# Optimization experiments

Hardware: AMD Instinct MI355X
Metric: run time of the kernel (lower is better)

The kernel has to match this reference:

```python
import jax, jax.numpy as jnp
import numpy as np

N, E = 30000, 240000          # nodes, edges per view
IN, D, OUT = 512, 128, 64      # in_dim, hidden_dim, out_dim
V, BLK, H, DM = 2, 2, 2, 64    # num_view, blk_size, num_heads, gate max-pool dim
NEG_ATT, NEG_OUT = 0.2, 0.01   # leaky_relu slopes (attention / outer)


def setup_inputs() -> dict:
    key = jax.random.key(0)
    ks = jax.random.split(key, 12)
    s = 0.05
    f32 = jnp.float32
    return {
        "ft": jax.random.normal(ks[0], (N, IN), f32),
        "src": jax.random.randint(ks[1], (V, E), 0, N, jnp.int32),
        "dst": jax.random.randint(ks[2], (V, E), 0, N, jnp.int32),
        "W_proj": jax.random.normal(ks[3], (IN, D), f32) * s,
        "W_embed": jax.random.normal(ks[4], (D, D), f32) * s,
        "a_l": jax.random.normal(ks[5], (V, BLK, H, D), f32) * s,
        "a_r": jax.random.normal(ks[6], (V, BLK, H, D), f32) * s,
        "Wv": jax.random.normal(ks[7], (V, BLK, H, D, D), f32) * s,
        "Wgm": jax.random.normal(ks[8], (V, BLK, D, DM), f32) * s,
        "Wgate": jax.random.normal(ks[9], (V, BLK, 2 * D + DM, H), f32) * s,
        "b_gate": jnp.zeros((V, BLK, H), f32),
        "W_tran": jax.random.normal(ks[10], (2 * D + DM and (D + V * H * D), OUT), f32) * s if False else jax.random.normal(ks[10], (D + V * H * D, OUT), f32) * s,
        "b_tran": jnp.zeros((OUT,), f32),
    }


def _seg_sum(x, idx):
    return jax.ops.segment_sum(x, idx, num_segments=N)


def _cgaan_layer(v, z, s_idx, d_idx, al, ar, wv, wgm, wgate, bg, merge):
    # v: [N,D] values, z: [N,D] attention features ('proj_z')
    # Multi-head attention logits: e_ij = leaky_relu(a_l.z_src + a_r.z_dst)  [E,H]
    logit_l = jnp.einsum("nd,hd->nh", z, al)
    logit_r = jnp.einsum("nd,hd->nh", z, ar)
    e = jax.nn.leaky_relu(logit_l[s_idx] + logit_r[d_idx], NEG_ATT)
    # edge softmax over incoming edges of each dst node
    m = jax.ops.segment_max(e, d_idx, num_segments=N)          # [N,H]
    ex = jnp.exp(e - m[d_idx])
    denom = _seg_sum(ex, d_idx)                                 # [N,H]
    alpha = ex / denom[d_idx]                                   # [E,H]
    # per-head value projection and weighted aggregation
    wvn = jnp.einsum("nd,hde->nhe", v, wv)                      # [N,H,D]
    agg = _seg_sum(alpha[:, :, None] * wvn[s_idx], d_idx)       # [N,H,D]
    # GaAN-style gate: sigmoid(FC([x_i, mean_j v_j, max_j (v_j Wgm)])) -> per-head scalar
    deg = _seg_sum(jnp.ones((s_idx.shape[0],), v.dtype), d_idx)  # [N]
    mean_n = _seg_sum(v[s_idx], d_idx) / jnp.maximum(deg, 1.0)[:, None]
    mx = jax.ops.segment_max((v @ wgm)[s_idx], d_idx, num_segments=N)
    mx = jnp.where(deg[:, None] > 0, mx, 0.0)                   # isolated nodes -> 0
    g = jax.nn.sigmoid(jnp.concatenate([v, mean_n, mx], -1) @ wgate + bg)  # [N,H]
    agg = g[:, :, None] * agg
    if merge == "mean":
        return agg.mean(axis=1)                                 # [N,D]
    return agg.reshape(agg.shape[0], -1)                        # cat -> [N,H*D]


def reference(ft, src, dst, W_proj, W_embed, a_l, a_r, Wv, Wgm, Wgate, b_gate, W_tran, b_tran):
    proj = ft @ W_proj                                          # [N,D]
    cur = [proj for _ in range(V)]
    for i in range(BLK):
        merge = "mean" if i < BLK - 1 else "cat"
        nxt = []
        for j in range(V):
            z = cur[j] @ W_embed
            h = _cgaan_layer(cur[j], z, src[j], dst[j], a_l[j, i], a_r[j, i],
                             Wv[j, i], Wgm[j, i], Wgate[j, i], b_gate[j, i], merge)
            nxt.append(jax.nn.leaky_relu(h, NEG_OUT))
        cur = nxt
    h = jnp.concatenate([proj] + cur, axis=-1)                  # [N, D+V*H*D]
    return h @ W_tran + b_tran
```

## Files before the change

### kernel.cpp

```cpp
#include <hip/hip_runtime.h>
#include <hip/hip_bf16.h>
#include <math.h>

#define NN 30000
#define EE 240000
#define IN_DIM 512
#define DD 128
#define OUTD 64
#define NV 2
#define NBLK 2
#define NH 2
#define DMM 64
#define NEG_ATT 0.2f
#define NEG_OUT 0.01f
#define CH 1024
#define NCH ((NN + CH - 1) / CH)

typedef __attribute__((ext_vector_type(8))) short bf16x8;
typedef __attribute__((ext_vector_type(4))) float f32x4;
typedef __attribute__((ext_vector_type(4))) unsigned short us4;
typedef __attribute__((ext_vector_type(8))) unsigned short us8;

#define OFF_PROJVM 0
#define OFF_WV     131072
#define OFF_WGM    262144
#define OFF_TRAN   278528
#define WT_TOTAL   319488

__device__ __forceinline__ unsigned split_bf(float x) {
  unsigned u = __float_as_uint(x);
  unsigned hb = (u + 0x7FFFu + ((u >> 16) & 1u)) >> 16;
  float hf = __uint_as_float(hb << 16);
  float lo = x - hf;
  unsigned ul = __float_as_uint(lo);
  unsigned lb = (ul + 0x7FFFu + ((ul >> 16) & 1u)) >> 16;
  return hb | (lb << 16);
}
__device__ __forceinline__ unsigned short f2bf(float x) {
  unsigned u = __float_as_uint(x);
  return (unsigned short)((u + 0x7FFFu + ((u >> 16) & 1u)) >> 16);
}
__device__ __forceinline__ float bf2f(unsigned short u) {
  return __uint_as_float((unsigned)u << 16);
}
__device__ __forceinline__ void gload16(void* lds, const void* g) {
  __builtin_amdgcn_global_load_lds((const __attribute__((address_space(1))) unsigned int*)g,
                                   (__attribute__((address_space(3))) unsigned int*)lds, 16, 0, 0);
}

__global__ __launch_bounds__(256) void kA_deg_prepw(const int* __restrict__ dst, int* __restrict__ deg,
                                                    const float* __restrict__ W_embed,
                                                    const float* __restrict__ a_l, const float* __restrict__ a_r,
                                                    const float* __restrict__ Wp, const float* __restrict__ Wgm,
                                                    float* __restrict__ Bl, float* __restrict__ Br,
                                                    float* __restrict__ wf) {
  int b = blockIdx.x;
  if (b < 1875) {
    int e = b * 256 + threadIdx.x;
    if (e < NV * EE) atomicAdd(&deg[(e / EE) * NN + dst[e]], 1);
    return;
  }
  int pb = b - 1875;
  if (pb < 256) {
    int idx = pb * 256 + threadIdx.x;
    int j = idx >> 15, k = (idx >> 6) & 511, n = idx & 63;
    const float* wp = Wp + (size_t)k * DD;
    const float* wg = Wgm + (size_t)(j * NBLK + 0) * DD * DMM + n;
    float s = 0.f;
    for (int e = 0; e < DD; e++) s += wp[e] * wg[(size_t)e * DMM];
    wf[idx] = s;
  } else {
    int idx = (pb - 256) * 256 + threadIdx.x;
    if (idx >= NV * NBLK * DD * NH) return;
    int h = idx & 1, dd = (idx >> 1) & 127, lv = idx >> 8;
    const float* w = W_embed + dd * DD;
    const float* al = a_l + (lv * NH + h) * DD;
    const float* ar = a_r + (lv * NH + h) * DD;
    float sl = 0.f, sr = 0.f;
    for (int e = 0; e < DD; e++) { float we = w[e]; sl += we * al[e]; sr += we * ar[e]; }
    Bl[idx] = sl; Br[idx] = sr;
  }
}

__global__ __launch_bounds__(256) void kB_scan1_wsplit(const int* __restrict__ deg, int* __restrict__ partial,
                                                       const float* __restrict__ Wp, const float* __restrict__ wf,
                                                       const float* __restrict__ Wv, const float* __restrict__ Wgm,
                                                       const float* __restrict__ Wt,
                                                       unsigned short* __restrict__ hi,
                                                       unsigned short* __restrict__ lo) {
  int b = blockIdx.x;
  if (b < 60) {
    int view = b / NCH, ch = b % NCH;
    const int* d = deg + view * NN + ch * CH;
    int rem = min(CH, NN - ch * CH);
    int t = threadIdx.x;
    int s = 0;
    for (int i = t; i < rem; i += 256) s += d[i];
    for (int k = 32; k; k >>= 1) s += __shfl_xor(s, k);
    __shared__ int wsum[4];
    if ((t & 63) == 0) wsum[t >> 6] = s;
    __syncthreads();
    if (t == 0) partial[b] = wsum[0] + wsum[1] + wsum[2] + wsum[3];
    return;
  }
  int wb = b - 60;
  const int pre[11] = {0, 256, 384, 512, 640, 768, 896, 1024, 1056, 1088, 1248};
  int y = 0;
  while (y < 10 && wb >= pre[y + 1]) y++;
  int bx = wb - pre[y];
  const float* src; int K, N; size_t doff;
  if (y == 0)      { src = Wp;                      K = 512; N = 128; doff = OFF_PROJVM; }
  else if (y <= 2) { int j = y - 1; src = wf + (size_t)j * 512 * 64; K = 512; N = 64; doff = OFF_PROJVM + (size_t)(128 + j * 64) * 512; }
  else if (y <= 6) { int lv = y - 3; src = Wv + (size_t)lv * 32768;  K = 256; N = 128; doff = OFF_WV + (size_t)lv * 32768; }
  else if (y <= 8) { int j = y - 7; src = Wgm + (size_t)(j * NBLK + 1) * 8192; K = 128; N = 64; doff = OFF_WGM + (size_t)j * 8192; }
  else             { src = Wt;                      K = 640; N = 64;  doff = OFF_TRAN; }
  int idx = bx * 256 + threadIdx.x;
  if (idx >= K * N) return;
  int n = idx / K, k = idx % K;
  int tk = k >> 6, g = (k >> 3) & 7, j2 = k & 7;
  int ks = (tk << 6) | ((g ^ (n & 7)) << 3) | j2;
  unsigned p = split_bf(src[(size_t)k * N + n]);
  hi[doff + (size_t)n * K + ks] = (unsigned short)(p & 0xFFFFu);
  lo[doff + (size_t)n * K + ks] = (unsigned short)(p >> 16);
}

__global__ void k_scan2(const int* __restrict__ partial, int* __restrict__ chunkoff, int* __restrict__ off) {
  if (threadIdx.x == 0 && blockIdx.x == 0) {
    for (int v = 0; v < NV; v++) {
      int acc = 0;
      for (int c = 0; c < NCH; c++) { chunkoff[v * NCH + c] = acc; acc += partial[v * NCH + c]; }
      off[v * (NN + 1) + NN] = acc;
    }
  }
}

__global__ __launch_bounds__(256) void k_scan3(const int* __restrict__ deg, const int* __restrict__ chunkoff,
                                               int* __restrict__ off) {
  int b = blockIdx.x, view = b / NCH, ch = b % NCH;
  int base = ch * CH;
  const int* d = deg + view * NN;
  int* o = off + view * (NN + 1);
  int t = threadIdx.x, lane = t & 63, w = t >> 6;
  int i0 = base + t * 4;
  int x0 = 0, x1 = 0, x2 = 0, x3 = 0;
  if (i0 + 3 < NN) { int4 q = *(const int4*)(d + i0); x0 = q.x; x1 = q.y; x2 = q.z; x3 = q.w; }
  else {
    if (i0     < NN) x0 = d[i0];
    if (i0 + 1 < NN) x1 = d[i0 + 1];
    if (i0 + 2 < NN) x2 = d[i0 + 2];
  }
  int tot = x0 + x1 + x2 + x3;
  int incl = tot;
  for (int k = 1; k < 64; k <<= 1) { int y = __shfl_up(incl, k); if (lane >= k) incl += y; }
  __shared__ int wt[4];
  if (lane == 63) wt[w] = incl;
  __syncthreads();
  int wexcl = 0;
  for (int k = 0; k < w; k++) wexcl += wt[k];
  int excl = chunkoff[b] + wexcl + incl - tot;
  if (i0     < NN) o[i0]     = excl;
  if (i0 + 1 < NN) o[i0 + 1] = excl + x0;
  if (i0 + 2 < NN) o[i0 + 2] = excl + x0 + x1;
  if (i0 + 3 < NN) o[i0 + 3] = excl + x0 + x1 + x2;
}

__global__ __launch_bounds__(256) void k_fill(const int* __restrict__ src, const int* __restrict__ dst,
                                              const int* __restrict__ off, int* __restrict__ cursor,
                                              int* __restrict__ csr_src) {
  int e = blockIdx.x * 256 + threadIdx.x;
  if (e >= NV * EE) return;
  int view = e / EE;
  int d = dst[e];
  int p = atomicAdd(&cursor[view * NN + d], 1);
  csr_src[view * EE + off[view * (NN + 1) + d] + p] = src[e];
}

__global__ __launch_bounds__(256) void k_llr(const unsigned short* __restrict__ p0,
                                             const unsigned short* __restrict__ p1, int ps,
                                             const float* __restrict__ Bl0, const float* __restrict__ Br0,
                                             const float* __restrict__ Bl1, const float* __restrict__ Br1,
                                             const float* __restrict__ Wg0, const float* __restrict__ Wg1,
                                             float4* __restrict__ lq, float2* __restrict__ lr) {
  int lane = threadIdx.x & 63, wid = threadIdx.x >> 6;
  int n = blockIdx.x * 4 + wid;
  int k = lane * 2;
  unsigned a = *(const unsigned*)(p0 + (size_t)n * ps + k);
  unsigned b = *(const unsigned*)(p1 + (size_t)n * ps + k);
  float ax = bf2f((unsigned short)a), ay = bf2f((unsigned short)(a >> 16));
  float bx = bf2f((unsigned short)b), by = bf2f((unsigned short)(b >> 16));
  float r[12];
  r[0]  = ax * Bl0[k * 2]     + ay * Bl0[k * 2 + 2];
  r[1]  = ax * Bl0[k * 2 + 1] + ay * Bl0[k * 2 + 3];
  r[2]  = ax * Br0[k * 2]     + ay * Br0[k * 2 + 2];
  r[3]  = ax * Br0[k * 2 + 1] + ay * Br0[k * 2 + 3];
  r[4]  = ax * Wg0[(128 + k) * 2]     + ay * Wg0[(129 + k) * 2];
  r[5]  = ax * Wg0[(128 + k) * 2 + 1] + ay * Wg0[(129 + k) * 2 + 1];
  r[6]  = bx * Bl1[k * 2]     + by * Bl1[k * 2 + 2];
  r[7]  = bx * Bl1[k * 2 + 1] + by * Bl1[k * 2 + 3];
  r[8]  = bx * Br1[k * 2]     + by * Br1[k * 2 + 2];
  r[9]  = bx * Br1[k * 2 + 1] + by * Br1[k * 2 + 3];
  r[10] = bx * Wg1[(128 + k) * 2]     + by * Wg1[(129 + k) * 2];
  r[11] = bx * Wg1[(128 + k) * 2 + 1] + by * Wg1[(129 + k) * 2 + 1];
  for (int s = 32; s; s >>= 1)
#pragma unroll
    for (int q = 0; q < 12; q++) r[q] += __shfl_xor(r[q], s);
  if (lane == 0) {
    lq[n] = make_float4(r[0], r[1], r[4], r[5]);
    lr[n] = make_float2(r[2], r[3]);
    lq[NN + n] = make_float4(r[6], r[7], r[10], r[11]);
    lr[NN + n] = make_float2(r[8], r[9]);
  }
}

__global__ __launch_bounds__(256) void k_edge(const int* __restrict__ off_, const int* __restrict__ csr_,
                                              const float4* __restrict__ lq_, const float2* __restrict__ lr_,
                                              const unsigned short* __restrict__ pk_, long viewStride,
                                              int ps, int vmoff0, int vmstep,
                                              const float* __restrict__ Wg_, const float* __restrict__ bg_,
                                              unsigned short* __restrict__ S_) {
  int view = blockIdx.y;
  const int* off = off_ + view * (NN + 1);
  const int* csr = csr_ + (size_t)view * EE;
  const float4* lq = lq_ + (size_t)view * NN;
  const float2* lrp = lr_ + (size_t)view * NN;
  const unsigned short* pk = pk_ + (size_t)view * viewStride;
  int vmoff = vmoff0 + view * vmstep;
  const float* Wg = Wg_ + (size_t)view * NBLK * (2 * DD + DMM) * NH;
  const float* bg = bg_ + view * NBLK * NH;
  unsigned short* S = S_ + (size_t)view * NN * 256;

  int lane = threadIdx.x & 63, wid = threadIdx.x >> 6;
  int n = blockIdx.x * 4 + wid;
  int e0 = off[n], nb = off[n + 1] - e0;
  int half = lane >> 5, hl = lane & 31;
  if (nb == 0) {
    us4 z4 = {0, 0, 0, 0};
    *(us4*)(S + (size_t)n * 256 + half * 128 + 4 * hl) = z4;
    return;
  }
  float2 lrn = lrp[n];
  float sa0[4] = {0.f, 0.f, 0.f, 0.f}, sa1[4] = {0.f, 0.f, 0.f, 0.f};
  float d0 = 0.f, d1 = 0.f, tm0 = 0.f, tm1 = 0.f, vm0 = -INFINITY, vm1 = -INFINITY;
  for (int base = 0; base < nb; base += 64) {
    int i = base + lane;
    float w0 = 0.f, w1 = 0.f; int sidx = 0;
    if (i < nb) {
      sidx = csr[e0 + i];
      float4 qq = lq[sidx];
      float x0 = qq.x + lrn.x, x1 = qq.y + lrn.y;
      x0 = (x0 > 0.f) ? x0 : NEG_ATT * x0;
      x1 = (x1 > 0.f) ? x1 : NEG_ATT * x1;
      w0 = __expf(x0); w1 = __expf(x1);
      d0 += w0; d1 += w1; tm0 += qq.z; tm1 += qq.w;
    }
    int cnt = min(64, nb - base);
    int steps = (cnt + 1) >> 1;
    int j = half;
    int se = __shfl(sidx, j);
    float wa = __shfl(w0, j), wb = __shfl(w1, j);
    const unsigned short* rp = pk + (size_t)se * ps;
    us4 vq = *(const us4*)(rp + 4 * hl);
    unsigned mu = *(const unsigned*)(rp + vmoff + 2 * hl);
    bool ok = (j < cnt);
    for (int s = 0; s < steps; s++) {
      int j1 = 2 * (s + 1) + half;
      int jc = min(j1, 63);
      int se1 = __shfl(sidx, jc);
      float wa1 = __shfl(w0, jc), wb1 = __shfl(w1, jc);
      const unsigned short* rp1 = pk + (size_t)se1 * ps;
      us4 vq1 = *(const us4*)(rp1 + 4 * hl);
      unsigned mu1 = *(const unsigned*)(rp1 + vmoff + 2 * hl);
      float v0 = bf2f(vq[0]), v1 = bf2f(vq[1]), v2 = bf2f(vq[2]), v3 = bf2f(vq[3]);
      sa0[0] += wa * v0; sa0[1] += wa * v1; sa0[2] += wa * v2; sa0[3] += wa * v3;
      sa1[0] += wb * v0; sa1[1] += wb * v1; sa1[2] += wb * v2; sa1[3] += wb * v3;
      float mv0 = ok ? bf2f((unsigned short)mu) : -INFINITY;
      float mv1 = ok ? bf2f((unsigned short)(mu >> 16)) : -INFINITY;
      vm0 = fmaxf(vm0, mv0); vm1 = fmaxf(vm1, mv1);
      vq = vq1; mu = mu1; wa = wa1; wb = wb1; ok = (j1 < cnt);
    }
  }
#pragma unroll
  for (int k = 0; k < 4; k++) {
    sa0[k] += __shfl_xor(sa0[k], 32);
    sa1[k] += __shfl_xor(sa1[k], 32);
  }
  vm0 = fmaxf(vm0, __shfl_xor(vm0, 32));
  vm1 = fmaxf(vm1, __shfl_xor(vm1, 32));
  for (int s = 32; s; s >>= 1) { d0 += __shfl_xor(d0, s); d1 += __shfl_xor(d1, s); }
  unsigned vnu = *(const unsigned*)(pk + (size_t)n * ps + 2 * lane);
  float vnx = bf2f((unsigned short)vnu), vny = bf2f((unsigned short)(vnu >> 16));
  float im = 1.f / (float)nb;
  float p0 = vnx * Wg[(2 * lane) * 2]     + vny * Wg[(2 * lane + 1) * 2]     + tm0 * im;
  float p1 = vnx * Wg[(2 * lane) * 2 + 1] + vny * Wg[(2 * lane + 1) * 2 + 1] + tm1 * im;
  if (half == 1) {
    p0 += vm0 * Wg[(256 + 2 * hl) * 2]     + vm1 * Wg[(256 + 2 * hl + 1) * 2];
    p1 += vm0 * Wg[(256 + 2 * hl) * 2 + 1] + vm1 * Wg[(256 + 2 * hl + 1) * 2 + 1];
  }
  for (int s = 32; s; s >>= 1) { p0 += __shfl_xor(p0, s); p1 += __shfl_xor(p1, s); }
  float g0 = 1.f / (1.f + __expf(-(p0 + bg[0])));
  float g1 = 1.f / (1.f + __expf(-(p1 + bg[1])));
  float q0 = g0 / d0, q1 = g1 / d1;
  us4 o4;
  if (half == 0) {
    o4[0] = f2bf(sa0[0] * q0); o4[1] = f2bf(sa0[1] * q0);
    o4[2] = f2bf(sa0[2] * q0); o4[3] = f2bf(sa0[3] * q0);
  } else {
    o4[0] = f2bf(sa1[0] * q1); o4[1] = f2bf(sa1[1] * q1);
    o4[2] = f2bf(sa1[2] * q1); o4[3] = f2bf(sa1[3] * q1);
  }
  *(us4*)(S + (size_t)n * 256 + half * 128 + 4 * hl) = o4;
}

struct GB {
  const void* A[4];
  unsigned long long bofs[4];
  float* C[4];
  unsigned short* P[4];
  int ldc[4];
  int pldc[4];
};

template <int BN, bool ABF>
__global__ __launch_bounds__(256) void gemm_mfma(
    GB gb, const unsigned short* __restrict__ Bth, const unsigned short* __restrict__ Btl,
    int lda, int ldb, int M, int K,
    const float* __restrict__ bias, float fs, int flags) {
  constexpr int NSUB = BN / 32;
  constexpr int CPW = BN / 32;
  __shared__ __align__(16) unsigned short Ah[64][64];
  __shared__ __align__(16) unsigned short Bh[BN][64], Bl[BN][64];
  const int z = blockIdx.z, xb = blockIdx.x;
  const float* __restrict__ Af = (const float*)gb.A[z];
  const unsigned short* __restrict__ Ab = (const unsigned short*)gb.A[z];
  float* __restrict__ C = gb.C[z];
  unsigned short* __restrict__ P = gb.P[z];
  const int ldc = gb.ldc[z], pldc = gb.pldc[z];
  const size_t bofs = gb.bofs[z];
  const int t = threadIdx.x;
  const int lane = t & 63, wv = t >> 6;
  const int lm = lane & 15, lg = lane >> 4;
  const int m0w = (wv & 1) * 32, n0w = (wv >> 1) * (BN / 2);
  const int row0 = xb * 64;
  f32x4 acc[2][NSUB];
#pragma unroll
  for (int ms = 0; ms < 2; ms++)
#pragma unroll
    for (int ns = 0; ns < NSUB; ns++) acc[ms][ns] = (f32x4)0.f;

  float4 apre[2][2];
  const int ar_ = t >> 3, ag_ = t & 7;

  auto loadA = [&](int k0) {
    if constexpr (!ABF) {
#pragma unroll
      for (int q = 0; q < 2; q++) {
        int rr = row0 + q * 32 + ar_;
        if (rr < M) {
          const float* p = Af + (size_t)rr * lda + k0 + ag_ * 8;
          apre[q][0] = *(const float4*)p;
          apre[q][1] = *(const float4*)(p + 4);
        } else {
          apre[q][0] = make_float4(0.f, 0.f, 0.f, 0.f);
          apre[q][1] = make_float4(0.f, 0.f, 0.f, 0.f);
        }
      }
    }
  };
  auto storeA = [&]() {
    if constexpr (!ABF) {
#pragma unroll
      for (int q = 0; q < 2; q++) {
        int r = q * 32 + ar_;
        us8 h8;
        float vals[8] = {apre[q][0].x, apre[q][0].y, apre[q][0].z, apre[q][0].w,
                         apre[q][1].x, apre[q][1].y, apre[q][1].z, apre[q][1].w};
#pragma unroll
        for (int e = 0; e < 8; e++) h8[e] = f2bf(vals[e]);
        int c = (ag_ ^ (r & 7)) << 3;
        *(us8*)&Ah[r][c] = h8;
      }
    }
  };
  auto stageA_bf = [&](int k0) {
    if constexpr (ABF) {
#pragma unroll
      for (int q = 0; q < 2; q++) {
        int r = q * 32 + ar_;
        int rr = min(row0 + r, M - 1);
        int scg = ag_ ^ (r & 7);
        gload16((char*)&Ah[0][0] + q * 4096 + t * 16,
                Ab + (size_t)rr * lda + k0 + scg * 8);
      }
    }
  };
  auto stageB = [&](int k0) {
#pragma unroll
    for (int q = 0; q < CPW; q++) {
      int chunk = wv * CPW + q;
      int o = chunk * 1024 + lane * 16;
      int n = o >> 7;
      int pq = (o >> 4) & 7;
      size_t gofs = bofs + (size_t)n * ldb + k0 + pq * 8;
      gload16((char*)&Bh[0][0] + o, Bth + gofs);
      gload16((char*)&Bl[0][0] + o, Btl + gofs);
    }
  };

  loadA(0);
  for (int k0 = 0; k0 < K; k0 += 64) {
    if constexpr (ABF) stageA_bf(k0); else storeA();
    stageB(k0);
    __syncthreads();
    if constexpr (!ABF) { if (k0 + 64 < K) loadA(k0 + 64); }
#pragma unroll
    for (int kc = 0; kc < 2; kc++) {
      bf16x8 afh[2], bfh[NSUB], bfl[NSUB];
#pragma unroll
      for (int ms = 0; ms < 2; ms++) {
        int R = m0w + ms * 16 + lm;
        int c = (((kc * 4 + lg) ^ (R & 7)) << 3);
        afh[ms] = *(const bf16x8*)&Ah[R][c];
      }
#pragma unroll
      for (int ns = 0; ns < NSUB; ns++) {
        int R = n0w + ns * 16 + lm;
        int c = (((kc * 4 + lg) ^ (R & 7)) << 3);
        bfh[ns] = *(const bf16x8*)&Bh[R][c];
        bfl[ns] = *(const bf16x8*)&Bl[R][c];
      }
#pragma unroll
      for (int ms = 0; ms < 2; ms++)
#pragma unroll
        for (int ns = 0; ns < NSUB; ns++) {
          acc[ms][ns] = __builtin_amdgcn_mfma_f32_16x16x32_bf16(afh[ms], bfl[ns], acc[ms][ns], 0, 0, 0);
          acc[ms][ns] = __builtin_amdgcn_mfma_f32_16x16x32_bf16(afh[ms], bfh[ns], acc[ms][ns], 0, 0, 0);
        }
    }
    __syncthreads();
  }
#pragma unroll
  for (int ms = 0; ms < 2; ms++)
#pragma unroll
    for (int ns = 0; ns < NSUB; ns++)
#pragma unroll
      for (int j = 0; j < 4; j++) {
        int row = row0 + m0w + ms * 16 + lg * 4 + j;
        if (row >= M) continue;
        int col = n0w + ns * 16 + lm;
        float val = acc[ms][ns][j] * fs;
        if (bias) val += bias[col];
        if (flags & 2) val = (val > 0.f) ? val : NEG_OUT * val;
        if (C) C[(size_t)row * ldc + col] = val;
        if (P) P[(size_t)row * pldc + col] = f2bf(val);
      }
}

extern "C" void kernel_launch(void* const* d_in, const int* in_sizes, int n_in,
                              void* d_out, int out_size, void* d_ws, size_t ws_size,
                              hipStream_t stream) {
  const float* ft      = (const float*)d_in[0];
  const int*   src     = (const int*)  d_in[1];
  const int*   dst     = (const int*)  d_in[2];
  const float* W_proj  = (const float*)d_in[3];
  const float* W_embed = (const float*)d_in[4];
  const float* a_l     = (const float*)d_in[5];
  const float* a_r     = (const float*)d_in[6];
  const float* Wv      = (const float*)d_in[7];
  const float* Wgm     = (const float*)d_in[8];
  const float* Wgate   = (const float*)d_in[9];
  const float* b_gate  = (const float*)d_in[10];
  const float* W_tran  = (const float*)d_in[11];
  const float* b_tran  = (const float*)d_in[12];
  float* out = (float*)d_out;
  char* ws = (char*)d_ws;
  (void)in_sizes; (void)n_in; (void)out_size; (void)ws_size;

  size_t o = 0;
  auto take = [&](size_t bytes) { size_t r = o; o += (bytes + 255) & ~(size_t)255; return r; };
  int*   deg     = (int*)(ws + take((size_t)NV * NN * 4));
  int*   cursor  = (int*)(ws + take((size_t)NV * NN * 4));
  int*   csr_off = (int*)(ws + take((size_t)NV * (NN + 1) * 4));
  int*   csr_src = (int*)(ws + take((size_t)NV * EE * 4));
  int*   partial = (int*)(ws + take((size_t)NV * NCH * 4));
  int*   chunkoff= (int*)(ws + take((size_t)NV * NCH * 4));
  float* Bl      = (float*)(ws + take((size_t)NV * NBLK * DD * NH * 4));
  float* Br      = (float*)(ws + take((size_t)NV * NBLK * DD * NH * 4));
  float* wf      = (float*)(ws + take((size_t)NV * 512 * 64 * 4));
  unsigned short* whi = (unsigned short*)(ws + take((size_t)WT_TOTAL * 2));
  unsigned short* wlo = (unsigned short*)(ws + take((size_t)WT_TOTAL * 2));
  float* h       = (float*)(ws + take((size_t)NN * 640 * 4));
  unsigned short* pk0 = (unsigned short*)(ws + take((size_t)NN * 256 * 2));
  unsigned short* pk1 = (unsigned short*)(ws + take((size_t)NV * NN * 192 * 2));
  unsigned short* Sbf = (unsigned short*)(ws + take((size_t)NV * NN * 256 * 2));
  float4* lqb    = (float4*)(ws + take((size_t)NV * NN * 16));
  float2* lrb    = (float2*)(ws + take((size_t)NV * NN * 8));

  const int HSTR = 640;

  hipMemsetAsync(deg, 0, (size_t)(((size_t)NV * NN * 4 + 255) & ~(size_t)255) + (size_t)NV * NN * 4, stream);
  kA_deg_prepw<<<2135, 256, 0, stream>>>(dst, deg, W_embed, a_l, a_r, W_proj, Wgm, Bl, Br, wf);
  kB_scan1_wsplit<<<1308, 256, 0, stream>>>(deg, partial, W_proj, wf, Wv, Wgm, W_tran, whi, wlo);
  k_scan2<<<1, 64, 0, stream>>>(partial, chunkoff, csr_off);
  k_scan3<<<NV * NCH, 256, 0, stream>>>(deg, chunkoff, csr_off);
  k_fill<<<(NV * EE + 255) / 256, 256, 0, stream>>>(src, dst, csr_off, cursor, csr_src);

  const int GM = (NN + 63) / 64;

  {
    GB gb = {};
    gb.A[0] = ft; gb.A[1] = ft;
    gb.bofs[0] = OFF_PROJVM; gb.bofs[1] = OFF_PROJVM + (size_t)128 * 512;
    gb.C[0] = h;  gb.ldc[0] = HSTR;
    gb.P[0] = pk0;       gb.pldc[0] = 256;
    gb.P[1] = pk0 + 128; gb.pldc[1] = 256;
    gemm_mfma<128, false><<<dim3(GM, 1, 2), 256, 0, stream>>>(gb, whi, wlo, IN_DIM, 512, NN, 512,
                                                              nullptr, 1.f, 0);
  }

  k_llr<<<NN / 4, 256, 0, stream>>>(pk0, pk0, 256,
                                    Bl + 0 * 256, Br + 0 * 256, Bl + 2 * 256, Br + 2 * 256,
                                    Wgate, Wgate + (size_t)NBLK * 320 * NH,
                                    lqb, lrb);
  k_edge<<<dim3(NN / 4, 2), 256, 0, stream>>>(csr_off, csr_src, lqb, lrb,
                                              pk0, 0L, 256, 128, 64,
                                              Wgate, b_gate, Sbf);
  {
    GB gb = {};
    for (int j = 0; j < 2; j++) {
      gb.A[j] = Sbf + (size_t)j * NN * 256;
      gb.bofs[j] = OFF_WV + (size_t)(j * 2) * 32768;
      gb.P[j] = pk1 + (size_t)j * NN * 192;
      gb.pldc[j] = 192;
    }
    gemm_mfma<128, true><<<dim3(GM, 1, 2), 256, 0, stream>>>(gb, whi, wlo, 256, 256, NN, 256,
                                                             nullptr, 0.5f, 2);
  }
  {
    GB gb = {};
    for (int j = 0; j < 2; j++) {
      gb.A[j] = pk1 + (size_t)j * NN * 192;
      gb.bofs[j] = OFF_WGM + (size_t)j * 8192;
      gb.P[j] = pk1 + (size_t)j * NN * 192 + 128;
      gb.pldc[j] = 192;
    }
    gemm_mfma<64, true><<<dim3(GM, 1, 2), 256, 0, stream>>>(gb, whi, wlo, 192, 128, NN, 128,
                                                            nullptr, 1.f, 0);
  }
  k_llr<<<NN / 4, 256, 0, stream>>>(pk1, pk1 + (size_t)NN * 192, 192,
                                    Bl + 1 * 256, Br + 1 * 256, Bl + 3 * 256, Br + 3 * 256,
                                    Wgate + 640, Wgate + (size_t)NBLK * 640 + 640,
                                    lqb, lrb);
  k_edge<<<dim3(NN / 4, 2), 256, 0, stream>>>(csr_off, csr_src, lqb, lrb,
                                              pk1, (long)NN * 192, 192, 128, 0,
                                              Wgate + 640, b_gate + NH, Sbf);
  {
    GB gb = {};
    for (int z = 0; z < 4; z++) {
      int j = z >> 1, hd = z & 1;
      gb.A[z] = Sbf + (size_t)j * NN * 256 + hd * 128;
      gb.bofs[z] = OFF_WV + (size_t)(j * 2 + 1) * 32768 + hd * 128;
      gb.C[z] = h + 128 + z * 128;
      gb.ldc[z] = HSTR;
    }
    gemm_mfma<128, true><<<dim3(GM, 1, 4), 256, 0, stream>>>(gb, whi, wlo, 256, 256, NN, 128,
                                                             nullptr, 1.f, 2);
  }
  {
    GB gb = {};
    gb.A[0] = h; gb.bofs[0] = OFF_TRAN; gb.C[0] = out; gb.ldc[0] = OUTD;
    gemm_mfma<64, false><<<dim3(GM, 1, 1), 256, 0, stream>>>(gb, whi, wlo, HSTR, 640, NN, 640,
                                                             b_tran, 1.f, 0);
  }
}
```

Before: 325.1 us.

## Fold CSR fill and logit kernels into GEMM launches and drop scan2

The single-thread chunk-offset scan kernel is removed. Each k_scan3 block now sums the partial counts of the preceding chunks itself and writes the final total. The CSR fill work is folded into extra blocks of the first projection GEMM, and the second attention-logit pass into extra blocks of the Wgm GEMM, selected by flag bits and block index. This cuts kernel launches and the serialization between small kernels, so the independent work can overlap with GEMM tiles. The edge kernel also precomputes byte offsets for the gathered rows to shave address arithmetic, at the cost of a larger GEMM kernel signature and early-exit branches in its blocks.

```diff
diff --git a/kernel.cpp b/kernel.cpp
--- a/kernel.cpp
+++ b/kernel.cpp
@@ -46,6 +46,55 @@
 __device__ __forceinline__ void gload16(void* lds, const void* g) {
   __builtin_amdgcn_global_load_lds((const __attribute__((address_space(1))) unsigned int*)g,
                                    (__attribute__((address_space(3))) unsigned int*)lds, 16, 0, 0);
+}
+
+struct AUX {
+  const int* fsrc; const int* fdst; const int* foff; int* fcur; int* fcsr;
+  const unsigned short* lp0; const unsigned short* lp1; int lps;
+  const float *lBl0, *lBr0, *lBl1, *lBr1, *lWg0, *lWg1;
+  float4* llq; float2* llr;
+};
+
+__device__ void fill_body(int fb, int t, const AUX& a) {
+  int e = fb * 256 + t;
+  if (e >= NV * EE) return;
+  int view = e / EE;
+  int d = a.fdst[e];
+  int p = atomicAdd(&a.fcur[view * NN + d], 1);
+  a.fcsr[view * EE + a.foff[view * (NN + 1) + d] + p] = a.fsrc[e];
+}
+
+__device__ void llr_body(int lid, int t, const AUX& a) {
+  int lane = t & 63, wid = t >> 6;
+  int n = lid * 4 + wid;
+  if (n >= NN) return;
+  int k = lane * 2;
+  unsigned av = *(const unsigned*)(a.lp0 + (size_t)n * a.lps + k);
+  unsigned bv = *(const unsigned*)(a.lp1 + (size_t)n * a.lps + k);
+  float ax = bf2f((unsigned short)av), ay = bf2f((unsigned short)(av >> 16));
+  float bx = bf2f((unsigned short)bv), by = bf2f((unsigned short)(bv >> 16));
+  float r[12];
+  r[0]  = ax * a.lBl0[k * 2]     + ay * a.lBl0[k * 2 + 2];
+  r[1]  = ax * a.lBl0[k * 2 + 1] + ay * a.lBl0[k * 2 + 3];
+  r[2]  = ax * a.lBr0[k * 2]     + ay * a.lBr0[k * 2 + 2];
+  r[3]  = ax * a.lBr0[k * 2 + 1] + ay * a.lBr0[k * 2 + 3];
+  r[4]  = ax * a.lWg0[(128 + k) * 2]     + ay * a.lWg0[(129 + k) * 2];
+  r[5]  = ax * a.lWg0[(128 + k) * 2 + 1] + ay * a.lWg0[(129 + k) * 2 + 1];
+  r[6]  = bx * a.lBl1[k * 2]     + by * a.lBl1[k * 2 + 2];
+  r[7]  = bx * a.lBl1[k * 2 + 1] + by * a.lBl1[k * 2 + 3];
+  r[8]  = bx * a.lBr1[k * 2]     + by * a.lBr1[k * 2 + 2];
+  r[9]  = bx * a.lBr1[k * 2 + 1] + by * a.lBr1[k * 2 + 3];
+  r[10] = bx * a.lWg1[(128 + k) * 2]     + by * a.lWg1[(129 + k) * 2];
+  r[11] = bx * a.lWg1[(128 + k) * 2 + 1] + by * a.lWg1[(129 + k) * 2 + 1];
+  for (int s = 32; s; s >>= 1)
+#pragma unroll
+    for (int q = 0; q < 12; q++) r[q] += __shfl_xor(r[q], s);
+  if (lane == 0) {
+    a.llq[n] = make_float4(r[0], r[1], r[4], r[5]);
+    a.llr[n] = make_float2(r[2], r[3]);
+    a.llq[NN + n] = make_float4(r[6], r[7], r[10], r[11]);
+    a.llr[NN + n] = make_float2(r[8], r[9]);
+  }
 }
 
 __global__ __launch_bounds__(256) void kA_deg_prepw(const int* __restrict__ dst, int* __restrict__ deg,
@@ -124,19 +173,11 @@
   lo[doff + (size_t)n * K + ks] = (unsigned short)(p >> 16);
 }
 
-__global__ void k_scan2(const int* __restrict__ partial, int* __restrict__ chunkoff, int* __restrict__ off) {
-  if (threadIdx.x == 0 && blockIdx.x == 0) {
-    for (int v = 0; v < NV; v++) {
-      int acc = 0;
-      for (int c = 0; c < NCH; c++) { chunkoff[v * NCH + c] = acc; acc += partial[v * NCH + c]; }
-      off[v * (NN + 1) + NN] = acc;
-    }
-  }
-}
-
-__global__ __launch_bounds__(256) void k_scan3(const int* __restrict__ deg, const int* __restrict__ chunkoff,
+__global__ __launch_bounds__(256) void k_scan3(const int* __restrict__ deg, const int* __restrict__ partial,
                                                int* __restrict__ off) {
   int b = blockIdx.x, view = b / NCH, ch = b % NCH;
+  int coff = 0;
+  for (int c = 0; c < ch; c++) coff += partial[view * NCH + c];
   int base = ch * CH;
   const int* d = deg + view * NN;
   int* o = off + view * (NN + 1);
@@ -157,59 +198,16 @@
   __syncthreads();
   int wexcl = 0;
   for (int k = 0; k < w; k++) wexcl += wt[k];
-  int excl = chunkoff[b] + wexcl + incl - tot;
+  int excl = coff + wexcl + incl - tot;
   if (i0     < NN) o[i0]     = excl;
   if (i0 + 1 < NN) o[i0 + 1] = excl + x0;
   if (i0 + 2 < NN) o[i0 + 2] = excl + x0 + x1;
   if (i0 + 3 < NN) o[i0 + 3] = excl + x0 + x1 + x2;
-}
-
-__global__ __launch_bounds__(256) void k_fill(const int* __restrict__ src, const int* __restrict__ dst,
-                                              const int* __restrict__ off, int* __restrict__ cursor,
-                                              int* __restrict__ csr_src) {
-  int e = blockIdx.x * 256 + threadIdx.x;
-  if (e >= NV * EE) return;
-  int view = e / EE;
-  int d = dst[e];
-  int p = atomicAdd(&cursor[view * NN + d], 1);
-  csr_src[view * EE + off[view * (NN + 1) + d] + p] = src[e];
-}
-
-__global__ __launch_bounds__(256) void k_llr(const unsigned short* __restrict__ p0,
-                                             const unsigned short* __restrict__ p1, int ps,
-                                             const float* __restrict__ Bl0, const float* __restrict__ Br0,
-                                             const float* __restrict__ Bl1, const float* __restrict__ Br1,
-                                             const float* __restrict__ Wg0, const float* __restrict__ Wg1,
-                                             float4* __restrict__ lq, float2* __restrict__ lr) {
-  int lane = threadIdx.x & 63, wid = threadIdx.x >> 6;
-  int n = blockIdx.x * 4 + wid;
-  int k = lane * 2;
-  unsigned a = *(const unsigned*)(p0 + (size_t)n * ps + k);
-  unsigned b = *(const unsigned*)(p1 + (size_t)n * ps + k);
-  float ax = bf2f((unsigned short)a), ay = bf2f((unsigned short)(a >> 16));
-  float bx = bf2f((unsigned short)b), by = bf2f((unsigned short)(b >> 16));
-  float r[12];
-  r[0]  = ax * Bl0[k * 2]     + ay * Bl0[k * 2 + 2];
-  r[1]  = ax * Bl0[k * 2 + 1] + ay * Bl0[k * 2 + 3];
-  r[2]  = ax * Br0[k * 2]     + ay * Br0[k * 2 + 2];
-  r[3]  = ax * Br0[k * 2 + 1] + ay * Br0[k * 2 + 3];
-  r[4]  = ax * Wg0[(128 + k) * 2]     + ay * Wg0[(129 + k) * 2];
-  r[5]  = ax * Wg0[(128 + k) * 2 + 1] + ay * Wg0[(129 + k) * 2 + 1];
-  r[6]  = bx * Bl1[k * 2]     + by * Bl1[k * 2 + 2];
-  r[7]  = bx * Bl1[k * 2 + 1] + by * Bl1[k * 2 + 3];
-  r[8]  = bx * Br1[k * 2]     + by * Br1[k * 2 + 2];
-  r[9]  = bx * Br1[k * 2 + 1] + by * Br1[k * 2 + 3];
-  r[10] = bx * Wg1[(128 + k) * 2]     + by * Wg1[(129 + k) * 2];
-  r[11] = bx * Wg1[(128 + k) * 2 + 1] + by * Wg1[(129 + k) * 2 + 1];
-  for (int s = 32; s; s >>= 1)
-#pragma unroll
-    for (int q = 0; q < 12; q++) r[q] += __shfl_xor(r[q], s);
-  if (lane == 0) {
-    lq[n] = make_float4(r[0], r[1], r[4], r[5]);
-    lr[n] = make_float2(r[2], r[3]);
-    lq[NN + n] = make_float4(r[6], r[7], r[10], r[11]);
-    lr[NN + n] = make_float2(r[8], r[9]);
-  }
+  if (ch == NCH - 1 && t == 0) o[NN] = coff + partial[b];
+}
+
+__global__ __launch_bounds__(256) void k_llr(AUX a) {
+  llr_body(blockIdx.x, threadIdx.x, a);
 }
 
 __global__ __launch_bounds__(256) void k_edge(const int* __restrict__ off_, const int* __restrict__ csr_,
@@ -224,7 +222,9 @@
   const float4* lq = lq_ + (size_t)view * NN;
   const float2* lrp = lr_ + (size_t)view * NN;
   const unsigned short* pk = pk_ + (size_t)view * viewStride;
-  int vmoff = vmoff0 + view * vmstep;
+  const char* pkc = (const char*)pk;
+  int psb = ps * 2;
+  int vmb = (vmoff0 + view * vmstep) * 2;
   const float* Wg = Wg_ + (size_t)view * NBLK * (2 * DD + DMM) * NH;
   const float* bg = bg_ + view * NBLK * NH;
   unsigned short* S = S_ + (size_t)view * NN * 256;
@@ -239,13 +239,16 @@
     return;
   }
   float2 lrn = lrp[n];
+  int voff = 8 * hl;
+  int moff = vmb + 4 * hl;
   float sa0[4] = {0.f, 0.f, 0.f, 0.f}, sa1[4] = {0.f, 0.f, 0.f, 0.f};
   float d0 = 0.f, d1 = 0.f, tm0 = 0.f, tm1 = 0.f, vm0 = -INFINITY, vm1 = -INFINITY;
   for (int base = 0; base < nb; base += 64) {
     int i = base + lane;
-    float w0 = 0.f, w1 = 0.f; int sidx = 0;
+    float w0 = 0.f, w1 = 0.f; unsigned boff = 0;
     if (i < nb) {
-      sidx = csr[e0 + i];
+      int sidx = csr[e0 + i];
+      boff = (unsigned)(sidx * psb);
       float4 qq = lq[sidx];
       float x0 = qq.x + lrn.x, x1 = qq.y + lrn.y;
       x0 = (x0 > 0.f) ? x0 : NEG_ATT * x0;
@@ -256,20 +259,18 @@
     int cnt = min(64, nb - base);
     int steps = (cnt + 1) >> 1;
     int j = half;
-    int se = __shfl(sidx, j);
+    unsigned bo = __shfl(boff, j);
     float wa = __shfl(w0, j), wb = __shfl(w1, j);
-    const unsigned short* rp = pk + (size_t)se * ps;
-    us4 vq = *(const us4*)(rp + 4 * hl);
-    unsigned mu = *(const unsigned*)(rp + vmoff + 2 * hl);
+    us4 vq = *(const us4*)(pkc + bo + voff);
+    unsigned mu = *(const unsigned*)(pkc + bo + moff);
     bool ok = (j < cnt);
     for (int s = 0; s < steps; s++) {
       int j1 = 2 * (s + 1) + half;
       int jc = min(j1, 63);
-      int se1 = __shfl(sidx, jc);
+      unsigned bo1 = __shfl(boff, jc);
       float wa1 = __shfl(w0, jc), wb1 = __shfl(w1, jc);
-      const unsigned short* rp1 = pk + (size_t)se1 * ps;
-      us4 vq1 = *(const us4*)(rp1 + 4 * hl);
-      unsigned mu1 = *(const unsigned*)(rp1 + vmoff + 2 * hl);
+      us4 vq1 = *(const us4*)(pkc + bo1 + voff);
+      unsigned mu1 = *(const unsigned*)(pkc + bo1 + moff);
       float v0 = bf2f(vq[0]), v1 = bf2f(vq[1]), v2 = bf2f(vq[2]), v3 = bf2f(vq[3]);
       sa0[0] += wa * v0; sa0[1] += wa * v1; sa0[2] += wa * v2; sa0[3] += wa * v3;
       sa1[0] += wb * v0; sa1[1] += wb * v1; sa1[2] += wb * v2; sa1[3] += wb * v3;
@@ -322,14 +323,23 @@
 
 template <int BN, bool ABF>
 __global__ __launch_bounds__(256) void gemm_mfma(
-    GB gb, const unsigned short* __restrict__ Bth, const unsigned short* __restrict__ Btl,
+    GB gb, AUX aux, const unsigned short* __restrict__ Bth, const unsigned short* __restrict__ Btl,
     int lda, int ldb, int M, int K,
     const float* __restrict__ bias, float fs, int flags) {
   constexpr int NSUB = BN / 32;
   constexpr int CPW = BN / 32;
   __shared__ __align__(16) unsigned short Ah[64][64];
   __shared__ __align__(16) unsigned short Bh[BN][64], Bl[BN][64];
-  const int z = blockIdx.z, xb = blockIdx.x;
+  int xb = blockIdx.x;
+  const int z = blockIdx.z;
+  if (flags & 8) {
+    if (xb < 938) { fill_body(xb + 938 * z, threadIdx.x, aux); return; }
+    xb -= 938;
+  }
+  if (flags & 16) {
+    if (xb < 3750) { llr_body(xb + 3750 * z, threadIdx.x, aux); return; }
+    xb -= 3750;
+  }
   const float* __restrict__ Af = (const float*)gb.A[z];
   const unsigned short* __restrict__ Ab = (const unsigned short*)gb.A[z];
   float* __restrict__ C = gb.C[z];
@@ -482,7 +492,6 @@
   int*   csr_off = (int*)(ws + take((size_t)NV * (NN + 1) * 4));
   int*   csr_src = (int*)(ws + take((size_t)NV * EE * 4));
   int*   partial = (int*)(ws + take((size_t)NV * NCH * 4));
-  int*   chunkoff= (int*)(ws + take((size_t)NV * NCH * 4));
   float* Bl      = (float*)(ws + take((size_t)NV * NBLK * DD * NH * 4));
   float* Br      = (float*)(ws + take((size_t)NV * NBLK * DD * NH * 4));
   float* wf      = (float*)(ws + take((size_t)NV * 512 * 64 * 4));
@@ -496,15 +505,12 @@
   float2* lrb    = (float2*)(ws + take((size_t)NV * NN * 8));
 
   const int HSTR = 640;
+  const int GM = (NN + 63) / 64;
 
   hipMemsetAsync(deg, 0, (size_t)(((size_t)NV * NN * 4 + 255) & ~(size_t)255) + (size_t)NV * NN * 4, stream);
   kA_deg_prepw<<<2135, 256, 0, stream>>>(dst, deg, W_embed, a_l, a_r, W_proj, Wgm, Bl, Br, wf);
   kB_scan1_wsplit<<<1308, 256, 0, stream>>>(deg, partial, W_proj, wf, Wv, Wgm, W_tran, whi, wlo);
-  k_scan2<<<1, 64, 0, stream>>>(partial, chunkoff, csr_off);
-  k_scan3<<<NV * NCH, 256, 0, stream>>>(deg, chunkoff, csr_off);
-  k_fill<<<(NV * EE + 255) / 256, 256, 0, stream>>>(src, dst, csr_off, cursor, csr_src);
-
-  const int GM = (NN + 63) / 64;
+  k_scan3<<<NV * NCH, 256, 0, stream>>>(deg, partial, csr_off);
 
   {
     GB gb = {};
@@ -513,14 +519,21 @@
     gb.C[0] = h;  gb.ldc[0] = HSTR;
     gb.P[0] = pk0;       gb.pldc[0] = 256;
     gb.P[1] = pk0 + 128; gb.pldc[1] = 256;
-    gemm_mfma<128, false><<<dim3(GM, 1, 2), 256, 0, stream>>>(gb, whi, wlo, IN_DIM, 512, NN, 512,
-                                                              nullptr, 1.f, 0);
-  }
-
-  k_llr<<<NN / 4, 256, 0, stream>>>(pk0, pk0, 256,
-                                    Bl + 0 * 256, Br + 0 * 256, Bl + 2 * 256, Br + 2 * 256,
-                                    Wgate, Wgate + (size_t)NBLK * 320 * NH,
-                                    lqb, lrb);
+    AUX ax = {};
+    ax.fsrc = src; ax.fdst = dst; ax.foff = csr_off; ax.fcur = cursor; ax.fcsr = csr_src;
+    gemm_mfma<128, false><<<dim3(938 + GM, 1, 2), 256, 0, stream>>>(gb, ax, whi, wlo, IN_DIM, 512,
+                                                                    NN, 512, nullptr, 1.f, 8);
+  }
+
+  {
+    AUX ax = {};
+    ax.lp0 = pk0; ax.lp1 = pk0; ax.lps = 256;
+    ax.lBl0 = Bl + 0 * 256; ax.lBr0 = Br + 0 * 256;
+    ax.lBl1 = Bl + 2 * 256; ax.lBr1 = Br + 2 * 256;
+    ax.lWg0 = Wgate; ax.lWg1 = Wgate + (size_t)NBLK * 320 * NH;
+    ax.llq = lqb; ax.llr = lrb;
+    k_llr<<<NN / 4, 256, 0, stream>>>(ax);
+  }
   k_edge<<<dim3(NN / 4, 2), 256, 0, stream>>>(csr_off, csr_src, lqb, lrb,
                                               pk0, 0L, 256, 128, 64,
                                               Wgate, b_gate, Sbf);
@@ -532,7 +545,8 @@
       gb.P[j] = pk1 + (size_t)j * NN * 192;
       gb.pldc[j] = 192;
     }
-    gemm_mfma<128, true><<<dim3(GM, 1, 2), 256, 0, stream>>>(gb, whi, wlo, 256, 256, NN, 256,
+    AUX ax = {};
+    gemm_mfma<128, true><<<dim3(GM, 1, 2), 256, 0, stream>>>(gb, ax, whi, wlo, 256, 256, NN, 256,
                                                              nullptr, 0.5f, 2);
   }
   {
@@ -543,13 +557,15 @@
       gb.P[j] = pk1 + (size_t)j * NN * 192 + 128;
       gb.pldc[j] = 192;
     }
-    gemm_mfma<64, true><<<dim3(GM, 1, 2), 256, 0, stream>>>(gb, whi, wlo, 192, 128, NN, 128,
-                                                            nullptr, 1.f, 0);
-  }
-  k_llr<<<NN / 4, 256, 0, stream>>>(pk1, pk1 + (size_t)NN * 192, 192,
-                                    Bl + 1 * 256, Br + 1 * 256, Bl + 3 * 256, Br + 3 * 256,
-                                    Wgate + 640, Wgate + (size_t)NBLK * 640 + 640,
-                                    lqb, lrb);
+    AUX ax = {};
+    ax.lp0 = pk1; ax.lp1 = pk1 + (size_t)NN * 192; ax.lps = 192;
+    ax.lBl0 = Bl + 1 * 256; ax.lBr0 = Br + 1 * 256;
+    ax.lBl1 = Bl + 3 * 256; ax.lBr1 = Br + 3 * 256;
+    ax.lWg0 = Wgate + 640; ax.lWg1 = Wgate + (size_t)NBLK * 640 + 640;
+    ax.llq = lqb; ax.llr = lrb;
+    gemm_mfma<64, true><<<dim3(3750 + GM, 1, 2), 256, 0, stream>>>(gb, ax, whi, wlo, 192, 128,
+                                                                   NN, 128, nullptr, 1.f, 16);
+  }
   k_edge<<<dim3(NN / 4, 2), 256, 0, stream>>>(csr_off, csr_src, lqb, lrb,
                                               pk1, (long)NN * 192, 192, 128, 0,
                                               Wgate + 640, b_gate + NH, Sbf);
@@ -562,13 +578,15 @@
       gb.C[z] = h + 128 + z * 128;
       gb.ldc[z] = HSTR;
     }
-    gemm_mfma<128, true><<<dim3(GM, 1, 4), 256, 0, stream>>>(gb, whi, wlo, 256, 256, NN, 128,
+    AUX ax = {};
+    gemm_mfma<128, true><<<dim3(GM, 1, 4), 256, 0, stream>>>(gb, ax, whi, wlo, 256, 256, NN, 128,
                                                              nullptr, 1.f, 2);
   }
   {
     GB gb = {};
     gb.A[0] = h; gb.bofs[0] = OFF_TRAN; gb.C[0] = out; gb.ldc[0] = OUTD;
-    gemm_mfma<64, false><<<dim3(GM, 1, 1), 256, 0, stream>>>(gb, whi, wlo, HSTR, 640, NN, 640,
+    AUX ax = {};
+    gemm_mfma<64, false><<<dim3(GM, 1, 1), 256, 0, stream>>>(gb, ax, whi, wlo, HSTR, 640, NN, 640,
                                                              b_tran, 1.f, 0);
   }
 }
```

Result: faster. 302.8 us (-6.9%).
